# Kernel optimization log

Hardware: AMD Instinct MI355X
Metric: run time of the kernel (lower is better)

Reference implementation:

```python
import jax, jax.numpy as jnp
import numpy as np

ROTARY = 32
MAX_POS = 10000

# Precompute complex rotary table exactly as the module does: rows are positions
# 0..9999 and the slice used is freqs_cis[-S:] (positions MAX_POS-S .. MAX_POS-1).
_ang = np.outer(np.arange(MAX_POS), 1.0 / 10000.0 ** (np.arange(0, ROTARY, 2) / ROTARY))
FREQS_CIS = jnp.asarray(np.cos(_ang) + 1j * np.sin(_ang), dtype=jnp.complex64)  # [MAX_POS, ROTARY//2]


def _apply_rotary(x):
    # x: [B, S, H, ROTARY]; split-half -> complex, multiply, interleave back.
    B, S, H, R = x.shape
    z = x.astype(jnp.float32).reshape(B, S, H, 2, R // 2)
    zc = jax.lax.complex(z[..., 0, :], z[..., 1, :])            # [B,S,H,R//2]
    zc = zc * FREQS_CIS[None, MAX_POS - S:, None, :]
    out = jnp.stack((jnp.real(zc), jnp.imag(zc)), axis=-1)       # [B,S,H,R//2,2] (interleaved)
    return out.reshape(B, S, H, R).astype(x.dtype)


def setup_inputs() -> dict:
    key = jax.random.key(0)
    ks = jax.random.split(key, 10)
    B, S, D, H, HD = 4, 1024, 4096, 32, 128
    scale = 0.02
    return {
        "x": jax.random.normal(ks[0], (B, S, D), dtype=jnp.float32),
        "attn_bias": jax.random.normal(ks[1], (1, 1, S, S), dtype=jnp.float32),
        "wq_kernel": jax.random.normal(ks[2], (D, H, HD), dtype=jnp.float32) * scale,
        "wq_bias": jax.random.normal(ks[3], (H, HD), dtype=jnp.float32) * scale,
        "wk_kernel": jax.random.normal(ks[4], (D, H, HD), dtype=jnp.float32) * scale,
        "wk_bias": jax.random.normal(ks[5], (H, HD), dtype=jnp.float32) * scale,
        "wv_kernel": jax.random.normal(ks[6], (D, H, HD), dtype=jnp.float32) * scale,
        "wv_bias": jax.random.normal(ks[7], (H, HD), dtype=jnp.float32) * scale,
        "wo_kernel": jax.random.normal(ks[8], (H, HD, D), dtype=jnp.float32) * scale,
        "wo_bias": jax.random.normal(ks[9], (D,), dtype=jnp.float32) * scale,
    }


def reference(x, attn_bias, wq_kernel, wq_bias, wk_kernel, wk_bias,
              wv_kernel, wv_bias, wo_kernel, wo_bias):
    # Projections (DenseGeneral -> [B, S, H, HD])
    q = jnp.einsum('bsd,dhk->bshk', x, wq_kernel) + wq_bias
    k = jnp.einsum('bsd,dhk->bshk', x, wk_kernel) + wk_bias
    v = jnp.einsum('bsd,dhk->bshk', x, wv_kernel) + wv_bias
    # Empty-cache prefill: update_cache just stores k/v unchanged.
    # Partial rotary on the first ROTARY channels.
    q = jnp.concatenate((_apply_rotary(q[..., :ROTARY]), q[..., ROTARY:]), axis=3)
    k = jnp.concatenate((_apply_rotary(k[..., :ROTARY]), k[..., ROTARY:]), axis=3)
    head_dim = k.shape[3]
    p = jnp.einsum('bqhd,bkhd->bhqk', q, k) / head_dim ** 0.5
    attn = jax.nn.softmax(p + attn_bias, axis=3)
    o = jnp.einsum('bhqk,bkhd->bqhd', attn, v)
    return jnp.einsum('bqhd,hdm->bqm', o, wo_kernel) + wo_bias
```

## Files before the change

kernel.cpp:

```cpp
#include <hip/hip_runtime.h>
#include <hip/hip_bf16.h>

typedef unsigned short u16;
typedef __attribute__((ext_vector_type(8))) short bf16x8;
typedef __attribute__((ext_vector_type(4))) float f32x4;

#define MFMA16(a, b, c) __builtin_amdgcn_mfma_f32_16x16x32_bf16((a), (b), (c), 0, 0, 0)

#define GLD16(src, dst)                                                        \
    __builtin_amdgcn_global_load_lds(                                          \
        (const __attribute__((address_space(1))) void*)(src),                  \
        (__attribute__((address_space(3))) void*)(dst), 16, 0, 0)

__device__ __forceinline__ float bf2f(u16 u) {
    union { unsigned int i; float f; } v;
    v.i = ((unsigned int)u) << 16;
    return v.f;
}
__device__ __forceinline__ u16 f2bf(float f) {
    unsigned int x = __float_as_uint(f);
    x += 0x7FFFu + ((x >> 16) & 1u);
    return (u16)(x >> 16);
}

__global__ void rope_table_kernel(float2* __restrict__ tab) {
    int i = blockIdx.x * 256 + threadIdx.x;
    if (i >= 1024 * 16) return;
    int s = i >> 4, p = i & 15;
    double ang = (double)(8976 + s) * pow(10000.0, -(double)p / 16.0);
    tab[i] = make_float2((float)cos(ang), (float)sin(ang));
}

__global__ __launch_bounds__(256) void xcast_kernel(const float* __restrict__ X,
                                                    u16* __restrict__ Xb, int n) {
    int i = (blockIdx.x * 256 + threadIdx.x) * 8;
    if (i >= n) return;
    float4 f0 = *(const float4*)(X + i);
    float4 f1 = *(const float4*)(X + i + 4);
    union { u16 u[8]; uint4 v; } o;
    o.u[0] = f2bf(f0.x); o.u[1] = f2bf(f0.y); o.u[2] = f2bf(f0.z); o.u[3] = f2bf(f0.w);
    o.u[4] = f2bf(f1.x); o.u[5] = f2bf(f1.y); o.u[6] = f2bf(f1.z); o.u[7] = f2bf(f1.w);
    *(uint4*)(Xb + i) = o.v;
}

__global__ __launch_bounds__(256) void wt_kernel(const float* __restrict__ W,
                                                 u16* __restrict__ WT, int K, int N) {
    __shared__ u16 t[64][72];
    const int kt = blockIdx.y * 64, nt = blockIdx.x * 64;
    const int tid = threadIdx.x;
#pragma unroll
    for (int i = 0; i < 4; i++) {
        int cid = tid + i * 256;
        int k = cid >> 4, c = cid & 15;
        float4 f = *(const float4*)(W + (size_t)(kt + k) * N + nt + c * 4);
        t[c * 4 + 0][k] = f2bf(f.x);
        t[c * 4 + 1][k] = f2bf(f.y);
        t[c * 4 + 2][k] = f2bf(f.z);
        t[c * 4 + 3][k] = f2bf(f.w);
    }
    __syncthreads();
#pragma unroll
    for (int i = 0; i < 2; i++) {
        int cid = tid + i * 256;
        int n = cid >> 3, c = cid & 7;
        union { u16 u[8]; uint4 v; } o;
#pragma unroll
        for (int j = 0; j < 8; j++) o.u[j] = t[n][c * 8 + j];
        *(uint4*)(WT + (size_t)(nt + n) * K + kt + c * 8) = o.v;
    }
}

__global__ __launch_bounds__(256) void vtrans_kernel(const u16* __restrict__ V,
                                                     u16* __restrict__ VT) {
    __shared__ u16 t[64][74];
    const int tid = threadIdx.x;
    const int bh = blockIdx.z;
    const int b = bh >> 5, h = bh & 31;
    const int s0 = blockIdx.x * 64, d0 = blockIdx.y * 64;
#pragma unroll
    for (int i = 0; i < 2; i++) {
        int c = tid + i * 256;
        int sr = c >> 3, dp = c & 7;
        union { u16 u[8]; uint4 v; } in;
        in.v = *(const uint4*)(V + (((size_t)b * 1024 + s0 + sr) * 32 + h) * 128 + d0 + dp * 8);
#pragma unroll
        for (int j = 0; j < 8; j++) t[dp * 8 + j][sr] = in.u[j];
    }
    __syncthreads();
#pragma unroll
    for (int i = 0; i < 2; i++) {
        int c = tid + i * 256;
        int dr = c >> 3, sp = c & 7;
        union { u16 u[8]; uint4 v; } o;
#pragma unroll
        for (int j = 0; j < 8; j++) o.u[j] = t[dr][sp * 8 + j];
        *(uint4*)(VT + (((size_t)b * 32 + h) * 128 + d0 + dr) * 1024 + s0 + sp * 8) = o.v;
    }
}

__global__ void rope_apply_kernel(u16* __restrict__ q, u16* __restrict__ k,
                                  const float2* __restrict__ tab) {
    int i = blockIdx.x * 256 + threadIdx.x;
    if (i >= 4 * 1024 * 32) return;
    int s = (i >> 5) & 1023;
    const float2* tp = tab + s * 16;
    u16* ptrs[2] = { q + (size_t)i * 128, k + (size_t)i * 128 };
#pragma unroll
    for (int t = 0; t < 2; t++) {
        u16* p = ptrs[t];
        u16 buf[32], outb[32];
        *(uint4*)(buf)      = *(const uint4*)(p);
        *(uint4*)(buf + 8)  = *(const uint4*)(p + 8);
        *(uint4*)(buf + 16) = *(const uint4*)(p + 16);
        *(uint4*)(buf + 24) = *(const uint4*)(p + 24);
#pragma unroll
        for (int j = 0; j < 16; j++) {
            float a = bf2f(buf[j]), b = bf2f(buf[j + 16]);
            float c = tp[j].x, sn = tp[j].y;
            outb[2 * j]     = f2bf(a * c - b * sn);
            outb[2 * j + 1] = f2bf(a * sn + b * c);
        }
        *(uint4*)(p)      = *(uint4*)(outb);
        *(uint4*)(p + 8)  = *(uint4*)(outb + 8);
        *(uint4*)(p + 16) = *(uint4*)(outb + 16);
        *(uint4*)(p + 24) = *(uint4*)(outb + 24);
    }
}

template<int OUT_F32>
__global__ __launch_bounds__(256) void gemm_bt_kernel(
    const u16* __restrict__ A, const u16* __restrict__ BT,
    const float* __restrict__ bias, void* __restrict__ Cv,
    int M, int N, int K) {
    constexpr int BK = 32;
    __shared__ u16 As[128 * BK];
    __shared__ u16 Bs[128 * BK];

    const int tid  = threadIdx.x;
    const int lane = tid & 63;
    const int wave = tid >> 6;
    const int quad = lane >> 4;
    const int lm   = lane & 15;
    const int m0 = blockIdx.y * 128;
    const int n0 = blockIdx.x * 128;
    const int wm = (wave >> 1) * 64;
    const int wn = (wave & 1) * 64;

    const f32x4 fz = {0.f, 0.f, 0.f, 0.f};
    f32x4 acc[4][4];
#pragma unroll
    for (int i = 0; i < 4; i++)
#pragma unroll
        for (int j = 0; j < 4; j++) acc[i][j] = fz;

    const int g0 = wave * 64 + lane;
    const int g1 = g0 + 256;
    const u16* aS0 = A  + (size_t)(m0 + (g0 >> 2)) * K + (g0 & 3) * 8;
    const u16* aS1 = A  + (size_t)(m0 + (g1 >> 2)) * K + (g1 & 3) * 8;
    const u16* bS0 = BT + (size_t)(n0 + (g0 >> 2)) * K + (g0 & 3) * 8;
    const u16* bS1 = BT + (size_t)(n0 + (g1 >> 2)) * K + (g1 & 3) * 8;
    u16* aD0 = As + (size_t)wave * 512;
    u16* aD1 = aD0 + 2048;
    u16* bD0 = Bs + (size_t)wave * 512;
    u16* bD1 = bD0 + 2048;

    for (int k0 = 0; k0 < K; k0 += BK) {
        GLD16(aS0 + k0, aD0);
        GLD16(aS1 + k0, aD1);
        GLD16(bS0 + k0, bD0);
        GLD16(bS1 + k0, bD1);
        __syncthreads();

        bf16x8 a[4], b[4];
#pragma unroll
        for (int i = 0; i < 4; i++)
            a[i] = *(const bf16x8*)(As + (wm + i * 16 + lm) * BK + quad * 8);
#pragma unroll
        for (int i = 0; i < 4; i++)
            b[i] = *(const bf16x8*)(Bs + (wn + i * 16 + lm) * BK + quad * 8);
#pragma unroll
        for (int i = 0; i < 4; i++)
#pragma unroll
            for (int j = 0; j < 4; j++)
                acc[i][j] = MFMA16(a[i], b[j], acc[i][j]);
        __syncthreads();
    }

#pragma unroll
    for (int j = 0; j < 4; j++) {
        int col = n0 + wn + j * 16 + lm;
        float bv = bias[col];
#pragma unroll
        for (int i = 0; i < 4; i++) {
            int rowb = m0 + wm + i * 16 + quad * 4;
#pragma unroll
            for (int r = 0; r < 4; r++) {
                float v = acc[i][j][r] + bv;
                if (OUT_F32) ((float*)Cv)[(size_t)(rowb + r) * N + col] = v;
                else         ((u16*)Cv)[(size_t)(rowb + r) * N + col] = f2bf(v);
            }
        }
    }
}

__global__ __launch_bounds__(256) void attn_kernel(
    const u16* __restrict__ Q, const u16* __restrict__ Kv,
    const u16* __restrict__ VT, const float* __restrict__ Bias,
    u16* __restrict__ O) {
    constexpr int S = 1024, H = 32, HD = 128;
    constexpr int PST = 72;
    __shared__ u16 Ks[64 * 128];
    __shared__ u16 Vst[128 * 64];
    __shared__ u16 Ps[4 * 16 * PST];

    const int tid  = threadIdx.x;
    const int lane = tid & 63;
    const int wave = tid >> 6;
    const int quad = lane >> 4;
    const int lm   = lane & 15;
    const int qt = blockIdx.x;
    const int h  = blockIdx.y;
    const int b  = blockIdx.z;
    const int qrow = qt * 64 + wave * 16;

    const u16* qb = Q + (((size_t)b * S + qrow + lm) * H + h) * HD;
    bf16x8 qf[4];
#pragma unroll
    for (int f = 0; f < 4; f++)
        qf[f] = *(const bf16x8*)(qb + f * 32 + quad * 8);

    const u16* kSrc[4];
    const u16* vSrc[4];
    u16* kDst[4];
    u16* vDst[4];
#pragma unroll
    for (int i = 0; i < 4; i++) {
        int g = i * 256 + wave * 64 + lane;
        int krow = g >> 4, kpart = (g & 15) ^ (krow & 7);
        kSrc[i] = Kv + (((size_t)b * S + krow) * H + h) * HD + kpart * 8;
        kDst[i] = Ks + (size_t)(i * 256 + wave * 64) * 8;
        int vrow = g >> 3, vpart = (g & 7) ^ (vrow & 7);
        vSrc[i] = VT + (((size_t)b * H + h) * HD + vrow) * S + vpart * 8;
        vDst[i] = Vst + (size_t)(i * 256 + wave * 64) * 8;
    }

    float m_run[4], l_run[4], alpha[4];
#pragma unroll
    for (int r = 0; r < 4; r++) { m_run[r] = -3.0e38f; l_run[r] = 0.f; }
    const f32x4 fz = {0.f, 0.f, 0.f, 0.f};
    f32x4 oacc[8];
#pragma unroll
    for (int t = 0; t < 8; t++) oacc[t] = fz;

    const float scale = 0.08838834764831845f;
    const int lx = lm & 7;

    for (int kt = 0; kt < S / 64; kt++) {
        const int key0 = kt * 64;
        const size_t kOff = (size_t)key0 * H * HD;
#pragma unroll
        for (int i = 0; i < 4; i++) GLD16(kSrc[i] + kOff, kDst[i]);
#pragma unroll
        for (int i = 0; i < 4; i++) GLD16(vSrc[i] + key0, vDst[i]);
        __syncthreads();

        f32x4 sc[4];
        __builtin_amdgcn_s_setprio(1);
#pragma unroll
        for (int kt2 = 0; kt2 < 4; kt2++) {
            f32x4 c = fz;
#pragma unroll
            for (int f = 0; f < 4; f++) {
                bf16x8 kf = *(const bf16x8*)(Ks + (kt2 * 16 + lm) * 128 + ((4 * f + quad) ^ lx) * 8);
                c = MFMA16(qf[f], kf, c);
            }
            sc[kt2] = c;
        }
        __builtin_amdgcn_s_setprio(0);

        bool need = false;
#pragma unroll
        for (int r = 0; r < 4; r++) {
            int qr = qrow + quad * 4 + r;
            const float* bp = Bias + (size_t)qr * S + key0 + lm;
            float s0 = sc[0][r] * scale + bp[0];
            float s1 = sc[1][r] * scale + bp[16];
            float s2 = sc[2][r] * scale + bp[32];
            float s3 = sc[3][r] * scale + bp[48];
            float mx = fmaxf(fmaxf(s0, s1), fmaxf(s2, s3));
#pragma unroll
            for (int d = 1; d < 16; d <<= 1) mx = fmaxf(mx, __shfl_xor(mx, d));
            if (mx > m_run[r]) {
                alpha[r] = __expf(m_run[r] - mx);
                m_run[r] = mx;
                need = true;
            } else {
                alpha[r] = 1.f;
            }
            float p0 = __expf(s0 - m_run[r]);
            float p1 = __expf(s1 - m_run[r]);
            float p2 = __expf(s2 - m_run[r]);
            float p3 = __expf(s3 - m_run[r]);
            float ps = (p0 + p1) + (p2 + p3);
#pragma unroll
            for (int d = 1; d < 16; d <<= 1) ps += __shfl_xor(ps, d);
            l_run[r] = l_run[r] * alpha[r] + ps;
            u16* pr = Ps + wave * (16 * PST) + (quad * 4 + r) * PST + lm;
            pr[0]  = f2bf(p0);
            pr[16] = f2bf(p1);
            pr[32] = f2bf(p2);
            pr[48] = f2bf(p3);
        }
        if (need) {
#pragma unroll
            for (int t = 0; t < 8; t++)
#pragma unroll
                for (int r = 0; r < 4; r++) oacc[t][r] *= alpha[r];
        }
        __syncthreads();

        bf16x8 pf0 = *(const bf16x8*)(Ps + wave * (16 * PST) + lm * PST + quad * 8);
        bf16x8 pf1 = *(const bf16x8*)(Ps + wave * (16 * PST) + lm * PST + 32 + quad * 8);
        __builtin_amdgcn_s_setprio(1);
#pragma unroll
        for (int t = 0; t < 8; t++) {
            bf16x8 vf0 = *(const bf16x8*)(Vst + (t * 16 + lm) * 64 + (quad ^ lx) * 8);
            bf16x8 vf1 = *(const bf16x8*)(Vst + (t * 16 + lm) * 64 + ((4 + quad) ^ lx) * 8);
            oacc[t] = MFMA16(pf0, vf0, oacc[t]);
            oacc[t] = MFMA16(pf1, vf1, oacc[t]);
        }
        __builtin_amdgcn_s_setprio(0);
        __syncthreads();
    }

    u16* ob = O + (((size_t)b * S + qrow) * H + h) * HD;
#pragma unroll
    for (int r = 0; r < 4; r++) {
        float inv = 1.0f / l_run[r];
#pragma unroll
        for (int t = 0; t < 8; t++) {
            int hd = t * 16 + lm;
            ob[(size_t)(quad * 4 + r) * H * HD + hd] = f2bf(oacc[t][r] * inv);
        }
    }
}

extern "C" void kernel_launch(void* const* d_in, const int* in_sizes, int n_in,
                              void* d_out, int out_size, void* d_ws, size_t ws_size,
                              hipStream_t stream) {
    const float* x   = (const float*)d_in[0];
    const float* ab  = (const float*)d_in[1];
    const float* wq  = (const float*)d_in[2];
    const float* wqb = (const float*)d_in[3];
    const float* wk  = (const float*)d_in[4];
    const float* wkb = (const float*)d_in[5];
    const float* wv  = (const float*)d_in[6];
    const float* wvb = (const float*)d_in[7];
    const float* wo  = (const float*)d_in[8];
    const float* wob = (const float*)d_in[9];
    float* out = (float*)d_out;

    const size_t MAT = (size_t)4096 * 4096;
    u16* qb = (u16*)d_ws;
    u16* kb = qb + MAT;
    u16* vb = kb + MAT;
    u16* ob = vb + MAT;
    u16* xb = ob + MAT;
    u16* wt = xb + MAT;
    float2* tab = (float2*)(wt + MAT);
    u16* vt = xb;

    rope_table_kernel<<<64, 256, 0, stream>>>(tab);
    xcast_kernel<<<8192, 256, 0, stream>>>(x, xb, (int)MAT);

    dim3 g(32, 32);
    dim3 wtg(64, 64);
    wt_kernel<<<wtg, 256, 0, stream>>>(wq, wt, 4096, 4096);
    gemm_bt_kernel<0><<<g, 256, 0, stream>>>(xb, wt, wqb, qb, 4096, 4096, 4096);
    wt_kernel<<<wtg, 256, 0, stream>>>(wk, wt, 4096, 4096);
    gemm_bt_kernel<0><<<g, 256, 0, stream>>>(xb, wt, wkb, kb, 4096, 4096, 4096);
    wt_kernel<<<wtg, 256, 0, stream>>>(wv, wt, 4096, 4096);
    gemm_bt_kernel<0><<<g, 256, 0, stream>>>(xb, wt, wvb, vb, 4096, 4096, 4096);

    rope_apply_kernel<<<512, 256, 0, stream>>>(qb, kb, tab);
    vtrans_kernel<<<dim3(16, 2, 128), 256, 0, stream>>>(vb, vt);
    attn_kernel<<<dim3(16, 32, 4), 256, 0, stream>>>(qb, kb, vt, ab, ob);

    wt_kernel<<<wtg, 256, 0, stream>>>(wo, wt, 4096, 4096);
    gemm_bt_kernel<1><<<g, 256, 0, stream>>>(ob, wt, wob, out, 4096, 4096, 4096);
}
```

Baseline: 1.395 ms.

## Load K/V fragments directly from global memory in attention and drop LDS staging

The attention kernel stops staging K and V tiles in shared memory via global_load_lds and removes the block-wide barriers. Each wave now reads its MFMA fragments straight from global memory and relies on L2 for reuse across waves and blocks. The block index is also remapped so that blocks sharing the same (batch, head) K/V are scheduled close together. The bias loads are hoisted ahead of the QK MFMAs, and the row-sum reduction is deferred to the end. The aim is to cut LDS traffic and synchronisation, at the cost of four times the global/L2 reads, since every wave fetches the full K/V tile.

```diff
diff --git a/kernel.cpp b/kernel.cpp
--- a/kernel.cpp
+++ b/kernel.cpp
@@ -209,8 +209,6 @@
     u16* __restrict__ O) {
     constexpr int S = 1024, H = 32, HD = 128;
     constexpr int PST = 72;
-    __shared__ u16 Ks[64 * 128];
-    __shared__ u16 Vst[128 * 64];
     __shared__ u16 Ps[4 * 16 * PST];
 
     const int tid  = threadIdx.x;
@@ -218,9 +216,13 @@
     const int wave = tid >> 6;
     const int quad = lane >> 4;
     const int lm   = lane & 15;
-    const int qt = blockIdx.x;
-    const int h  = blockIdx.y;
-    const int b  = blockIdx.z;
+
+    const int L = blockIdx.x + 16 * (blockIdx.y + 32 * blockIdx.z);
+    const int i2 = L >> 3;
+    const int qt = i2 & 15;
+    const int pair = (L & 7) * 16 + (i2 >> 4);
+    const int h = pair & 31;
+    const int b = pair >> 5;
     const int qrow = qt * 64 + wave * 16;
 
     const u16* qb = Q + (((size_t)b * S + qrow + lm) * H + h) * HD;
@@ -229,40 +231,32 @@
     for (int f = 0; f < 4; f++)
         qf[f] = *(const bf16x8*)(qb + f * 32 + quad * 8);
 
-    const u16* kSrc[4];
-    const u16* vSrc[4];
-    u16* kDst[4];
-    u16* vDst[4];
-#pragma unroll
-    for (int i = 0; i < 4; i++) {
-        int g = i * 256 + wave * 64 + lane;
-        int krow = g >> 4, kpart = (g & 15) ^ (krow & 7);
-        kSrc[i] = Kv + (((size_t)b * S + krow) * H + h) * HD + kpart * 8;
-        kDst[i] = Ks + (size_t)(i * 256 + wave * 64) * 8;
-        int vrow = g >> 3, vpart = (g & 7) ^ (vrow & 7);
-        vSrc[i] = VT + (((size_t)b * H + h) * HD + vrow) * S + vpart * 8;
-        vDst[i] = Vst + (size_t)(i * 256 + wave * 64) * 8;
-    }
-
-    float m_run[4], l_run[4], alpha[4];
-#pragma unroll
-    for (int r = 0; r < 4; r++) { m_run[r] = -3.0e38f; l_run[r] = 0.f; }
+    const u16* kL = Kv + (((size_t)b * S + lm) * H + h) * HD + quad * 8;
+    const u16* vL = VT + (((size_t)b * H + h) * HD + lm) * S + quad * 8;
+    const float* bL = Bias + (size_t)(qrow + quad * 4) * S + lm;
+
+    float m_run[4], l_lane[4], alpha[4];
+#pragma unroll
+    for (int r = 0; r < 4; r++) { m_run[r] = -3.0e38f; l_lane[r] = 0.f; }
     const f32x4 fz = {0.f, 0.f, 0.f, 0.f};
     f32x4 oacc[8];
 #pragma unroll
     for (int t = 0; t < 8; t++) oacc[t] = fz;
 
     const float scale = 0.08838834764831845f;
-    const int lx = lm & 7;
 
     for (int kt = 0; kt < S / 64; kt++) {
         const int key0 = kt * 64;
-        const size_t kOff = (size_t)key0 * H * HD;
-#pragma unroll
-        for (int i = 0; i < 4; i++) GLD16(kSrc[i] + kOff, kDst[i]);
-#pragma unroll
-        for (int i = 0; i < 4; i++) GLD16(vSrc[i] + key0, vDst[i]);
-        __syncthreads();
+
+        float bias_r[4][4];
+#pragma unroll
+        for (int r = 0; r < 4; r++) {
+            const float* bp = bL + (size_t)r * S + key0;
+            bias_r[r][0] = bp[0];
+            bias_r[r][1] = bp[16];
+            bias_r[r][2] = bp[32];
+            bias_r[r][3] = bp[48];
+        }
 
         f32x4 sc[4];
         __builtin_amdgcn_s_setprio(1);
@@ -271,7 +265,7 @@
             f32x4 c = fz;
 #pragma unroll
             for (int f = 0; f < 4; f++) {
-                bf16x8 kf = *(const bf16x8*)(Ks + (kt2 * 16 + lm) * 128 + ((4 * f + quad) ^ lx) * 8);
+                bf16x8 kf = *(const bf16x8*)(kL + (size_t)(key0 + kt2 * 16) * (H * HD) + f * 32);
                 c = MFMA16(qf[f], kf, c);
             }
             sc[kt2] = c;
@@ -281,12 +275,10 @@
         bool need = false;
 #pragma unroll
         for (int r = 0; r < 4; r++) {
-            int qr = qrow + quad * 4 + r;
-            const float* bp = Bias + (size_t)qr * S + key0 + lm;
-            float s0 = sc[0][r] * scale + bp[0];
-            float s1 = sc[1][r] * scale + bp[16];
-            float s2 = sc[2][r] * scale + bp[32];
-            float s3 = sc[3][r] * scale + bp[48];
+            float s0 = sc[0][r] * scale + bias_r[r][0];
+            float s1 = sc[1][r] * scale + bias_r[r][1];
+            float s2 = sc[2][r] * scale + bias_r[r][2];
+            float s3 = sc[3][r] * scale + bias_r[r][3];
             float mx = fmaxf(fmaxf(s0, s1), fmaxf(s2, s3));
 #pragma unroll
             for (int d = 1; d < 16; d <<= 1) mx = fmaxf(mx, __shfl_xor(mx, d));
@@ -301,10 +293,7 @@
             float p1 = __expf(s1 - m_run[r]);
             float p2 = __expf(s2 - m_run[r]);
             float p3 = __expf(s3 - m_run[r]);
-            float ps = (p0 + p1) + (p2 + p3);
-#pragma unroll
-            for (int d = 1; d < 16; d <<= 1) ps += __shfl_xor(ps, d);
-            l_run[r] = l_run[r] * alpha[r] + ps;
+            l_lane[r] = l_lane[r] * alpha[r] + ((p0 + p1) + (p2 + p3));
             u16* pr = Ps + wave * (16 * PST) + (quad * 4 + r) * PST + lm;
             pr[0]  = f2bf(p0);
             pr[16] = f2bf(p1);
@@ -317,26 +306,27 @@
 #pragma unroll
                 for (int r = 0; r < 4; r++) oacc[t][r] *= alpha[r];
         }
-        __syncthreads();
 
         bf16x8 pf0 = *(const bf16x8*)(Ps + wave * (16 * PST) + lm * PST + quad * 8);
         bf16x8 pf1 = *(const bf16x8*)(Ps + wave * (16 * PST) + lm * PST + 32 + quad * 8);
         __builtin_amdgcn_s_setprio(1);
 #pragma unroll
         for (int t = 0; t < 8; t++) {
-            bf16x8 vf0 = *(const bf16x8*)(Vst + (t * 16 + lm) * 64 + (quad ^ lx) * 8);
-            bf16x8 vf1 = *(const bf16x8*)(Vst + (t * 16 + lm) * 64 + ((4 + quad) ^ lx) * 8);
+            bf16x8 vf0 = *(const bf16x8*)(vL + (size_t)(t * 16) * S + key0);
+            bf16x8 vf1 = *(const bf16x8*)(vL + (size_t)(t * 16) * S + key0 + 32);
             oacc[t] = MFMA16(pf0, vf0, oacc[t]);
             oacc[t] = MFMA16(pf1, vf1, oacc[t]);
         }
         __builtin_amdgcn_s_setprio(0);
-        __syncthreads();
     }
 
     u16* ob = O + (((size_t)b * S + qrow) * H + h) * HD;
 #pragma unroll
     for (int r = 0; r < 4; r++) {
-        float inv = 1.0f / l_run[r];
+        float ls = l_lane[r];
+#pragma unroll
+        for (int d = 1; d < 16; d <<= 1) ls += __shfl_xor(ls, d);
+        float inv = 1.0f / ls;
 #pragma unroll
         for (int t = 0; t < 8; t++) {
             int hd = t * 16 + lm;
```

After: 1.682 ms. +20.6%, slower.
